# Kernel optimization log

Measured on AMD Instinct MI355X. Metric: run time of the kernel, lower is better.

## Reference

```python
import jax, jax.numpy as jnp
import numpy as np

SIGMA = 1.0   # kernel influence distance (init kwarg)
RADIUS = 1.0  # kernel radius (kernel points live within this ball)


def setup_inputs() -> dict:
    key = jax.random.key(0)
    k0, k1, k2, k3, k4, k5 = jax.random.split(key, 6)
    N, M, H, K, Cin, Cout = 50000, 50000, 32, 15, 64, 64
    q_points = jax.random.normal(k0, (M, 3), dtype=jnp.float32)
    s_points = jax.random.normal(k1, (N, 3), dtype=jnp.float32)
    s_feats = jax.random.normal(k2, (N, Cin), dtype=jnp.float32)
    # index == N selects the padded 'fantom' point (zero features, far away)
    neighbor_indices = jax.random.randint(k3, (M, H), 0, N + 1, dtype=jnp.int64)
    kernel_points = jax.random.normal(k4, (K, 3), dtype=jnp.float32) * (0.4 * RADIUS)
    weights = jax.random.normal(k5, (K, Cin, Cout), dtype=jnp.float32) * 0.05
    return {
        'q_points': q_points,
        's_points': s_points,
        's_feats': s_feats,
        'neighbor_indices': neighbor_indices,
        'kernel_points': kernel_points,
        'weights': weights,
    }


def reference(q_points, s_points, s_feats, neighbor_indices, kernel_points, weights):
    # Pad source points with a far-away fantom point and zero features so that
    # neighbor_indices == N behaves as an empty neighbor slot.
    s_pts = jnp.concatenate([s_points, jnp.full((1, 3), 1e6, s_points.dtype)], axis=0)
    s_fts = jnp.concatenate([s_feats, jnp.zeros((1, s_feats.shape[1]), s_feats.dtype)], axis=0)

    # Gather neighbors and center on query points: (M, H, 3)
    neighbors = s_pts[neighbor_indices] - q_points[:, None, :]
    # Distances to each kernel point: (M, H, K)
    diffs = neighbors[:, :, None, :] - kernel_points[None, None, :, :]
    sq_dists = jnp.sum(diffs * diffs, axis=-1)
    # Linear kernel influence (KPConv 'linear' mode): (M, H, K)
    influence = jnp.maximum(1.0 - jnp.sqrt(sq_dists) / SIGMA, 0.0)
    # Fantom neighbors are ~1e6 away -> influence exactly 0.

    # Gather neighbor features: (M, H, Cin)
    nb_feats = s_fts[neighbor_indices]
    # Weight features by kernel influence, reduce over neighbors: (M, K, Cin)
    weighted = jnp.einsum('mhk,mhc->mkc', influence, nb_feats)
    # Apply per-kernel-point linear maps and sum over kernel points: (M, Cout)
    out = jnp.einsum('mkc,kcd->md', weighted, weights)

    # Normalize by the number of valid (non-zero-feature) neighbors.
    feat_sum = jnp.sum(nb_feats, axis=-1)               # (M, H)
    nnum = jnp.maximum(jnp.sum(feat_sum > 0.0, axis=-1), 1)  # (M,)
    return out / nnum[:, None].astype(out.dtype)
```

## Files before the change

kernel.cpp:

```cpp
#include <hip/hip_runtime.h>

#define NPTS 50000
#define MPTS 50000
#define HN 32
#define KCD 960
#define PSTRIDE 968
#define FSTRIDE 40

typedef float f32x4 __attribute__((ext_vector_type(4)));
typedef short s16x8 __attribute__((ext_vector_type(8)));

__device__ __forceinline__ unsigned short bf_rne(float x) {
    union { float f; unsigned u; } v; v.f = x;
    unsigned r = v.u + 0x7fffu + ((v.u >> 16) & 1u);
    return (unsigned short)(r >> 16);
}
__device__ __forceinline__ unsigned short bf_trunc(float x) {
    union { float f; unsigned u; } v; v.f = x;
    return (unsigned short)(v.u >> 16);
}

__global__ __launch_bounds__(256) void prep(const float* __restrict__ w,
                                            const float* __restrict__ feats,
                                            unsigned short* __restrict__ WT,
                                            unsigned char* __restrict__ signs) {
    int b = blockIdx.x;
    if (b < 240) {
        int t = b * 256 + threadIdx.x;
        int d = t / 960, kc = t - d * 960;
        int k = kc >> 6, c = kc & 63;
        WT[t] = bf_rne(w[(k * 64 + c) * 64 + d]);
    } else {
        int n = (b - 240) * 256 + threadIdx.x;
        if (n < NPTS) {
            const float4* fp = (const float4*)(feats + (size_t)n * 64);
            float s = 0.f;
            #pragma unroll
            for (int j = 0; j < 16; ++j) { float4 v = fp[j]; s += v.x + v.y + v.z + v.w; }
            signs[n] = (s > 0.f) ? 1 : 0;
        }
    }
}

__global__ __launch_bounds__(256, 3)
void kpconv_main(const float* __restrict__ q_points,
                 const float* __restrict__ s_points,
                 const float* __restrict__ s_feats,
                 const int* __restrict__ ni,
                 const float* __restrict__ kpts,
                 const unsigned short* __restrict__ WT,
                 const unsigned char* __restrict__ signs,
                 float* __restrict__ out) {
    __shared__ __align__(16) unsigned short P_sh[16][PSTRIDE];
    __shared__ __align__(16) unsigned short feats_sh[4][64][FSTRIDE];
    __shared__ __align__(16) float rpos_sh[4][3][32];
    __shared__ float kp_sh[16][3];
    __shared__ float q_sh[16][3];
    __shared__ float inv_nnum[16];

    int tid = threadIdx.x, w = tid >> 6, lane = tid & 63;
    int m_base = blockIdx.x << 4;

    if (tid < 48) {
        kp_sh[tid / 3][tid % 3] = (tid < 45) ? kpts[tid] : 1e9f;
        q_sh[tid / 3][tid % 3] = q_points[m_base * 3 + tid];
    }
    __syncthreads();

    int h = lane & 31;
    int row = lane & 15, quad = lane >> 4, kq = quad << 3;

    float kx = kp_sh[row][0], ky = kp_sh[row][1], kz = kp_sh[row][2];

    float maxn2 = 0.f;
    #pragma unroll
    for (int k = 0; k < 15; ++k) {
        float a = kp_sh[k][0], b = kp_sh[k][1], c = kp_sh[k][2];
        maxn2 = fmaxf(maxn2, a * a + b * b + c * c);
    }
    float R0 = 1.f + sqrtf(maxn2);
    float R0sq = R0 * R0;

    int idx4[4]; float ppx[4], ppy[4], ppz[4]; unsigned char sg4[4];
    #pragma unroll
    for (int mi = 0; mi < 4; ++mi)
        idx4[mi] = ni[(m_base + mi * 4 + w) * HN + h];
    #pragma unroll
    for (int mi = 0; mi < 4; ++mi) {
        bool valid = idx4[mi] < NPTS;
        const float* sp = s_points + (size_t)(valid ? idx4[mi] : 0) * 3;
        float px = sp[0], py = sp[1], pz = sp[2];
        unsigned char sg = signs[valid ? idx4[mi] : 0];
        ppx[mi] = valid ? px : 1e6f;
        ppy[mi] = valid ? py : 1e6f;
        ppz[mi] = valid ? pz : 1e6f;
        sg4[mi] = valid ? sg : 0;
    }

    #pragma unroll
    for (int mi = 0; mi < 4; ++mi) {
        int m_l = mi * 4 + w;
        float rx = ppx[mi] - q_sh[m_l][0];
        float ry = ppy[mi] - q_sh[m_l][1];
        float rz = ppz[mi] - q_sh[m_l][2];
        if (lane < 32) {
            rpos_sh[w][0][h] = rx; rpos_sh[w][1][h] = ry; rpos_sh[w][2][h] = rz;
        }

        unsigned long long pm = __ballot((lane < 32) && (idx4[mi] < NPTS) && sg4[mi]);
        if (lane == 0) {
            int cnt = __popcll(pm);
            inv_nnum[m_l] = 1.f / (float)(cnt < 1 ? 1 : cnt);
        }

        int h2 = lane >> 1, half = lane & 1;
        float rx2 = __shfl(rx, h2), ry2 = __shfl(ry, h2), rz2 = __shfl(rz, h2);
        int idx2 = __shfl(idx4[mi], h2);
        bool alive2 = (idx2 < NPTS) && (rx2 * rx2 + ry2 * ry2 + rz2 * rz2 < R0sq);

        float4 fv[8];
        #pragma unroll
        for (int j = 0; j < 8; ++j) fv[j] = float4{0.f, 0.f, 0.f, 0.f};
        if (alive2) {
            const float4* fp = (const float4*)(s_feats + (size_t)idx2 * 64 + half * 32);
            #pragma unroll
            for (int j = 0; j < 8; ++j) { int jj = (j + half) & 7; fv[j] = fp[jj]; }
        }

        float4 ra0 = *(const float4*)&rpos_sh[w][0][kq];
        float4 ra1 = *(const float4*)&rpos_sh[w][0][kq + 4];
        float4 rb0 = *(const float4*)&rpos_sh[w][1][kq];
        float4 rb1 = *(const float4*)&rpos_sh[w][1][kq + 4];
        float4 rc0 = *(const float4*)&rpos_sh[w][2][kq];
        float4 rc1 = *(const float4*)&rpos_sh[w][2][kq + 4];
        float hx[8] = {ra0.x, ra0.y, ra0.z, ra0.w, ra1.x, ra1.y, ra1.z, ra1.w};
        float hy[8] = {rb0.x, rb0.y, rb0.z, rb0.w, rb1.x, rb1.y, rb1.z, rb1.w};
        float hz[8] = {rc0.x, rc0.y, rc0.z, rc0.w, rc1.x, rc1.y, rc1.z, rc1.w};
        s16x8 afrag;
        #pragma unroll
        for (int j = 0; j < 8; ++j) {
            float dx = hx[j] - kx, dy = hy[j] - ky, dz = hz[j] - kz;
            float d2 = dx * dx + dy * dy + dz * dz;
            float infl = 1.f - sqrtf(d2);
            infl = infl > 0.f ? infl : 0.f;
            afrag[j] = (short)bf_trunc(infl);
        }

        #pragma unroll
        for (int j = 0; j < 8; ++j) {
            int jj = (j + half) & 7;
            int c = half * 32 + jj * 4;
            float4 v = fv[j];
            feats_sh[w][c + 0][h2] = bf_trunc(v.x);
            feats_sh[w][c + 1][h2] = bf_trunc(v.y);
            feats_sh[w][c + 2][h2] = bf_trunc(v.z);
            feats_sh[w][c + 3][h2] = bf_trunc(v.w);
        }

        #pragma unroll
        for (int ch = 0; ch < 4; ++ch) {
            s16x8 bfrag = *(const s16x8*)&feats_sh[w][ch * 16 + row][kq];
            f32x4 acc = {0.f, 0.f, 0.f, 0.f};
            acc = __builtin_amdgcn_mfma_f32_16x16x32_bf16(afrag, bfrag, acc, 0, 0, 0);
            int cc = ch * 16 + row;
            #pragma unroll
            for (int r = 0; r < 4; ++r) {
                int k2 = quad * 4 + r;
                if (k2 < 15) {
                    int col = (k2 << 6) | (cc ^ ((k2 >> 2) << 4));
                    P_sh[m_l][col] = bf_trunc(acc[r]);
                }
            }
        }
    }
    __syncthreads();

    {
        int dbase = w << 4;
        f32x4 acc = {0.f, 0.f, 0.f, 0.f};
        const unsigned short* wtp = WT + (size_t)(dbase + row) * KCD + kq;
        #pragma unroll 6
        for (int s = 0; s < 30; ++s) {
            int k = s >> 1;
            int c0 = ((s & 1) << 5) + kq;
            int cx = c0 ^ (((k >> 2) & 3) << 4);
            s16x8 a = *(const s16x8*)&P_sh[row][(k << 6) | cx];
            s16x8 b = *(const s16x8*)&wtp[s * 32];
            acc = __builtin_amdgcn_mfma_f32_16x16x32_bf16(a, b, acc, 0, 0, 0);
        }
        #pragma unroll
        for (int r = 0; r < 4; ++r) {
            int m_l = quad * 4 + r;
            out[(size_t)(m_base + m_l) * 64 + dbase + row] = acc[r] * inv_nnum[m_l];
        }
    }
}

extern "C" void kernel_launch(void* const* d_in, const int* in_sizes, int n_in,
                              void* d_out, int out_size, void* d_ws, size_t ws_size,
                              hipStream_t stream) {
    const float* q  = (const float*)d_in[0];
    const float* sp = (const float*)d_in[1];
    const float* sf = (const float*)d_in[2];
    const int*   ni = (const int*)d_in[3];
    const float* kp = (const float*)d_in[4];
    const float* wt = (const float*)d_in[5];
    float* out = (float*)d_out;

    unsigned short* WT = (unsigned short*)d_ws;
    unsigned char* signs = (unsigned char*)d_ws + 64 * KCD * 2;

    hipLaunchKernelGGL(prep, dim3(240 + (NPTS + 255) / 256), dim3(256), 0, stream,
                       wt, sf, WT, signs);
    hipLaunchKernelGGL(kpconv_main, dim3(MPTS / 16), dim3(256), 0, stream,
                       q, sp, sf, ni, kp, WT, signs, out);
}
```

Before: 166.5 us.

## Double-buffer neighbor feature loads, tighten alive test, coalesce prep kernel

The main kernel now precomputes relative positions and a per-neighbor alive flag, testing against each of the 15 kernel points (split across lane pairs) instead of a bounding radius. This skips feature gathers for neighbors that influence no kernel point. Feature loads for the next query are issued one iteration ahead into a second register buffer, so gather latency overlaps the MFMA and LDS work of the current query. The prep kernel reads weights coalesced and computes feature-sign sums with 16 lanes per point plus shuffles, at the cost of more registers and more prep blocks.

```diff
diff --git a/kernel.cpp b/kernel.cpp
--- a/kernel.cpp
+++ b/kernel.cpp
@@ -27,18 +27,17 @@
     int b = blockIdx.x;
     if (b < 240) {
         int t = b * 256 + threadIdx.x;
-        int d = t / 960, kc = t - d * 960;
-        int k = kc >> 6, c = kc & 63;
-        WT[t] = bf_rne(w[(k * 64 + c) * 64 + d]);
+        int kc = t >> 6, d = t & 63;
+        WT[d * KCD + kc] = bf_rne(w[t]);
     } else {
-        int n = (b - 240) * 256 + threadIdx.x;
-        if (n < NPTS) {
-            const float4* fp = (const float4*)(feats + (size_t)n * 64);
-            float s = 0.f;
-            #pragma unroll
-            for (int j = 0; j < 16; ++j) { float4 v = fp[j]; s += v.x + v.y + v.z + v.w; }
-            signs[n] = (s > 0.f) ? 1 : 0;
-        }
+        int lane = threadIdx.x & 63, wv = threadIdx.x >> 6;
+        int r4 = lane >> 4, c16 = lane & 15;
+        int n = (b - 240) * 16 + wv * 4 + r4;
+        float4 v = *(const float4*)(feats + (size_t)n * 64 + c16 * 4);
+        float s = v.x + v.y + v.z + v.w;
+        s += __shfl_xor(s, 1); s += __shfl_xor(s, 2);
+        s += __shfl_xor(s, 4); s += __shfl_xor(s, 8);
+        if (c16 == 0) signs[n] = (s > 0.f) ? 1 : 0;
     }
 }
 
@@ -69,62 +68,87 @@
 
     int h = lane & 31;
     int row = lane & 15, quad = lane >> 4, kq = quad << 3;
+    int h2 = lane >> 1, half = lane & 1;
 
     float kx = kp_sh[row][0], ky = kp_sh[row][1], kz = kp_sh[row][2];
 
-    float maxn2 = 0.f;
-    #pragma unroll
-    for (int k = 0; k < 15; ++k) {
-        float a = kp_sh[k][0], b = kp_sh[k][1], c = kp_sh[k][2];
-        maxn2 = fmaxf(maxn2, a * a + b * b + c * c);
-    }
-    float R0 = 1.f + sqrtf(maxn2);
-    float R0sq = R0 * R0;
-
-    int idx4[4]; float ppx[4], ppy[4], ppz[4]; unsigned char sg4[4];
+    float tkx[8], tky[8], tkz[8];
+    #pragma unroll
+    for (int j = 0; j < 8; ++j) {
+        int k = half * 8 + j;
+        tkx[j] = kp_sh[k][0]; tky[j] = kp_sh[k][1]; tkz[j] = kp_sh[k][2];
+    }
+
+    int idx4[4]; float rxa[4], rya[4], rza[4]; unsigned char sg4[4];
     #pragma unroll
     for (int mi = 0; mi < 4; ++mi)
         idx4[mi] = ni[(m_base + mi * 4 + w) * HN + h];
     #pragma unroll
     for (int mi = 0; mi < 4; ++mi) {
+        int m_l = mi * 4 + w;
         bool valid = idx4[mi] < NPTS;
         const float* sp = s_points + (size_t)(valid ? idx4[mi] : 0) * 3;
         float px = sp[0], py = sp[1], pz = sp[2];
         unsigned char sg = signs[valid ? idx4[mi] : 0];
-        ppx[mi] = valid ? px : 1e6f;
-        ppy[mi] = valid ? py : 1e6f;
-        ppz[mi] = valid ? pz : 1e6f;
+        rxa[mi] = (valid ? px : 1e6f) - q_sh[m_l][0];
+        rya[mi] = (valid ? py : 1e6f) - q_sh[m_l][1];
+        rza[mi] = (valid ? pz : 1e6f) - q_sh[m_l][2];
         sg4[mi] = valid ? sg : 0;
     }
 
+    bool alive2[4]; int idx2c[4];
     #pragma unroll
     for (int mi = 0; mi < 4; ++mi) {
+        float rx2 = __shfl(rxa[mi], h2);
+        float ry2 = __shfl(rya[mi], h2);
+        float rz2 = __shfl(rza[mi], h2);
+        int idx2 = __shfl(idx4[mi], h2);
+        int av = 0;
+        #pragma unroll
+        for (int j = 0; j < 8; ++j) {
+            float dx = rx2 - tkx[j], dy = ry2 - tky[j], dz = rz2 - tkz[j];
+            float d2 = dx * dx + dy * dy + dz * dz;
+            av |= (d2 < 1.f) ? 1 : 0;
+        }
+        av |= __shfl_xor(av, 1);
+        alive2[mi] = (idx2 < NPTS) && (av != 0);
+        idx2c[mi] = idx2 < NPTS ? idx2 : 0;
+    }
+
+    float4 fv[2][8];
+    #define ISSUE(buf, mi)                                                        \
+        {                                                                         \
+            _Pragma("unroll")                                                     \
+            for (int j = 0; j < 8; ++j) fv[buf][j] = float4{0.f, 0.f, 0.f, 0.f};  \
+            if (alive2[mi]) {                                                     \
+                const float4* fp =                                                \
+                    (const float4*)(s_feats + (size_t)idx2c[mi] * 64 + half * 32);\
+                _Pragma("unroll")                                                 \
+                for (int j = 0; j < 8; ++j) {                                     \
+                    int jj = (j + half) & 7;                                      \
+                    fv[buf][j] = fp[jj];                                          \
+                }                                                                 \
+            }                                                                     \
+        }
+
+    ISSUE(0, 0)
+
+    #pragma unroll
+    for (int mi = 0; mi < 4; ++mi) {
+        int cur = mi & 1;
+        if (mi < 3) { ISSUE(1 - cur, mi + 1) }
+
         int m_l = mi * 4 + w;
-        float rx = ppx[mi] - q_sh[m_l][0];
-        float ry = ppy[mi] - q_sh[m_l][1];
-        float rz = ppz[mi] - q_sh[m_l][2];
         if (lane < 32) {
-            rpos_sh[w][0][h] = rx; rpos_sh[w][1][h] = ry; rpos_sh[w][2][h] = rz;
+            rpos_sh[w][0][h] = rxa[mi];
+            rpos_sh[w][1][h] = rya[mi];
+            rpos_sh[w][2][h] = rza[mi];
         }
 
         unsigned long long pm = __ballot((lane < 32) && (idx4[mi] < NPTS) && sg4[mi]);
         if (lane == 0) {
             int cnt = __popcll(pm);
             inv_nnum[m_l] = 1.f / (float)(cnt < 1 ? 1 : cnt);
-        }
-
-        int h2 = lane >> 1, half = lane & 1;
-        float rx2 = __shfl(rx, h2), ry2 = __shfl(ry, h2), rz2 = __shfl(rz, h2);
-        int idx2 = __shfl(idx4[mi], h2);
-        bool alive2 = (idx2 < NPTS) && (rx2 * rx2 + ry2 * ry2 + rz2 * rz2 < R0sq);
-
-        float4 fv[8];
-        #pragma unroll
-        for (int j = 0; j < 8; ++j) fv[j] = float4{0.f, 0.f, 0.f, 0.f};
-        if (alive2) {
-            const float4* fp = (const float4*)(s_feats + (size_t)idx2 * 64 + half * 32);
-            #pragma unroll
-            for (int j = 0; j < 8; ++j) { int jj = (j + half) & 7; fv[j] = fp[jj]; }
         }
 
         float4 ra0 = *(const float4*)&rpos_sh[w][0][kq];
@@ -150,7 +174,7 @@
         for (int j = 0; j < 8; ++j) {
             int jj = (j + half) & 7;
             int c = half * 32 + jj * 4;
-            float4 v = fv[j];
+            float4 v = fv[cur][j];
             feats_sh[w][c + 0][h2] = bf_trunc(v.x);
             feats_sh[w][c + 1][h2] = bf_trunc(v.y);
             feats_sh[w][c + 2][h2] = bf_trunc(v.z);
@@ -210,7 +234,7 @@
     unsigned short* WT = (unsigned short*)d_ws;
     unsigned char* signs = (unsigned char*)d_ws + 64 * KCD * 2;
 
-    hipLaunchKernelGGL(prep, dim3(240 + (NPTS + 255) / 256), dim3(256), 0, stream,
+    hipLaunchKernelGGL(prep, dim3(240 + NPTS / 16), dim3(256), 0, stream,
                        wt, sf, WT, signs);
     hipLaunchKernelGGL(kpconv_main, dim3(MPTS / 16), dim3(256), 0, stream,
                        q, sp, sf, ni, kp, WT, signs, out);
```

Result: no change. 164.2 us (-1.4%).
